# Optimization experiments

Measured on AMD Instinct MI355X. Metric: run time of the kernel, lower is better.

## Reference

```python
import jax, jax.numpy as jnp
import numpy as np

D_MODEL = 1024
N_HEADS = 16
D_HEAD = D_MODEL // N_HEADS
D_FF = 4 * D_MODEL
SEQ = 2048
BATCH = 4
EPS = 1e-5


def setup_inputs() -> dict:
    key = jax.random.key(0)
    ks = jax.random.split(key, 12)
    s = 0.02
    return {
        "x": jax.random.normal(ks[0], (BATCH, SEQ, D_MODEL), dtype=jnp.float32),
        "ln1_g": jnp.ones((D_MODEL,), jnp.float32),
        "ln1_b": jnp.zeros((D_MODEL,), jnp.float32),
        "wq": jax.random.normal(ks[1], (N_HEADS, D_MODEL, D_HEAD), jnp.float32) * s,
        "bq": jnp.zeros((N_HEADS, D_HEAD), jnp.float32),
        "wk": jax.random.normal(ks[2], (N_HEADS, D_MODEL, D_HEAD), jnp.float32) * s,
        "bk": jnp.zeros((N_HEADS, D_HEAD), jnp.float32),
        "wv": jax.random.normal(ks[3], (N_HEADS, D_MODEL, D_HEAD), jnp.float32) * s,
        "bv": jnp.zeros((N_HEADS, D_HEAD), jnp.float32),
        "wp": jax.random.normal(ks[4], (D_MODEL, D_MODEL), jnp.float32) * s,
        "bp": jnp.zeros((D_MODEL,), jnp.float32),
        "ln2_g": jnp.ones((D_MODEL,), jnp.float32),
        "ln2_b": jnp.zeros((D_MODEL,), jnp.float32),
        "w1": jax.random.normal(ks[5], (D_MODEL, D_FF), jnp.float32) * s,
        "b1": jnp.zeros((D_FF,), jnp.float32),
        "w2": jax.random.normal(ks[6], (D_FF, D_MODEL), jnp.float32) * s,
        "b2": jnp.zeros((D_MODEL,), jnp.float32),
    }


def _layer_norm(x, g, b):
    mu = jnp.mean(x, axis=-1, keepdims=True)
    var = jnp.mean(jnp.square(x - mu), axis=-1, keepdims=True)
    return (x - mu) * jax.lax.rsqrt(var + EPS) * g + b


def _block(x, ln1_g, ln1_b, wq, bq, wk, bk, wv, bv, wp, bp,
           ln2_g, ln2_b, w1, b1, w2, b2):
    B, S, D = x.shape
    # --- pre-LN multi-head causal self-attention ---
    xn = _layer_norm(x, ln1_g, ln1_b)
    q = jnp.einsum('bsd,hde->bhse', xn, wq) + bq[None, :, None, :]
    k = jnp.einsum('bsd,hde->bhse', xn, wk) + bk[None, :, None, :]
    v = jnp.einsum('bsd,hde->bhse', xn, wv) + bv[None, :, None, :]
    scores = jnp.einsum('bhse,bhte->bhst', q, k) / np.sqrt(D_HEAD).astype(np.float32)
    causal = jnp.tril(jnp.ones((S, S), dtype=bool))
    scores = jnp.where(causal[None, None], scores, jnp.float32(-jnp.inf))
    attn = jax.nn.softmax(scores, axis=-1)
    o = jnp.einsum('bhst,bhte->bhse', attn, v)          # [B,H,S,Dh]
    o = o.transpose(0, 2, 1, 3).reshape(B, S, D)         # concat heads
    x = x + o @ wp + bp
    # --- pre-LN feedforward ---
    xn2 = _layer_norm(x, ln2_g, ln2_b)
    h = jax.nn.relu(xn2 @ w1 + b1)
    x = x + h @ w2 + b2
    return x


def reference(x, ln1_g, ln1_b, wq, bq, wk, bk, wv, bv, wp, bp,
              ln2_g, ln2_b, w1, b1, w2, b2):
    return _block(x, ln1_g, ln1_b, wq, bq, wk, bk, wv, bv, wp, bp,
                  ln2_g, ln2_b, w1, b1, w2, b2)
```

## Files before the change

kernel.cpp:

```cpp
#include <hip/hip_runtime.h>
#include <hip/hip_bf16.h>

#define D_MODEL 1024
#define N_HEADS 16
#define D_HEAD  64
#define D_FF    4096
#define SEQ     2048
#define BATCH   4
#define NROWS   (BATCH * SEQ)

typedef __attribute__((ext_vector_type(8))) short short8;
typedef __attribute__((ext_vector_type(4))) float f32x4;

#define EXP2(x) exp2f(x)
#define MFMA16(a, b, c) __builtin_amdgcn_mfma_f32_16x16x32_bf16(a, b, c, 0, 0, 0)

static __device__ __forceinline__ ushort f2bf(float x) {
  __hip_bfloat16 h = __float2bfloat16(x);
  return *reinterpret_cast<ushort*>(&h);
}

static __device__ __forceinline__ void gl_lds16(const ushort* g, ushort* l) {
  __builtin_amdgcn_global_load_lds(
      (const __attribute__((address_space(1))) void*)g,
      (__attribute__((address_space(3))) void*)l, 16, 0, 0);
}

__global__ __launch_bounds__(256) void transpose_pack_b(
    const float* __restrict__ in, ushort* __restrict__ out,
    int K, int N, size_t in_bs, size_t out_bs) {
  in  += (size_t)blockIdx.z * in_bs;
  out += (size_t)blockIdx.z * out_bs;
  __shared__ float tile[32][33];
  int n0 = blockIdx.x * 32, k0 = blockIdx.y * 32;
  int tx = threadIdx.x, ty = threadIdx.y;
#pragma unroll
  for (int i = 0; i < 32; i += 8)
    tile[ty + i][tx] = in[(size_t)(k0 + ty + i) * N + n0 + tx];
  __syncthreads();
#pragma unroll
  for (int i = 0; i < 32; i += 8)
    out[(size_t)(n0 + ty + i) * K + k0 + tx] = f2bf(tile[tx][ty + i]);
}

__global__ __launch_bounds__(256) void transpose_v(
    const ushort* __restrict__ v, ushort* __restrict__ vt) {
  const int s0 = blockIdx.x * 64;
  const int bh = blockIdx.y, bb = bh >> 4, hh = bh & 15;
  __shared__ ushort tile[64][66];
  const ushort* src = v + (size_t)bb * SEQ * D_MODEL + (size_t)hh * 64;
  const int tx = threadIdx.x;
#pragma unroll
  for (int i = threadIdx.y; i < 64; i += 4)
    tile[i][tx] = src[(size_t)(s0 + i) * D_MODEL + tx];
  __syncthreads();
  ushort* dst = vt + (size_t)bh * 64 * SEQ + s0;
#pragma unroll
  for (int d = threadIdx.y; d < 64; d += 4)
    dst[(size_t)d * SEQ + tx] = tile[tx][d];
}

__global__ __launch_bounds__(256) void ln_kernel(
    const float* __restrict__ x, const float* __restrict__ g,
    const float* __restrict__ b, ushort* __restrict__ out) {
  int row = blockIdx.x, t = threadIdx.x;
  const float4 v = *(const float4*)(x + (size_t)row * D_MODEL + t * 4);
  float s  = v.x + v.y + v.z + v.w;
  float ss = v.x * v.x + v.y * v.y + v.z * v.z + v.w * v.w;
#pragma unroll
  for (int off = 1; off < 64; off <<= 1) {
    s  += __shfl_xor(s, off, 64);
    ss += __shfl_xor(ss, off, 64);
  }
  __shared__ float rs_[4], rss_[4];
  int w = t >> 6;
  if ((t & 63) == 0) { rs_[w] = s; rss_[w] = ss; }
  __syncthreads();
  s  = rs_[0] + rs_[1] + rs_[2] + rs_[3];
  ss = rss_[0] + rss_[1] + rss_[2] + rss_[3];
  float mu  = s * (1.0f / D_MODEL);
  float var = ss * (1.0f / D_MODEL) - mu * mu;
  float rstd = rsqrtf(var + 1e-5f);
  float4 gg = *(const float4*)(g + t * 4);
  float4 bb = *(const float4*)(b + t * 4);
  ushort4 r;
  r.x = f2bf((v.x - mu) * rstd * gg.x + bb.x);
  r.y = f2bf((v.y - mu) * rstd * gg.y + bb.y);
  r.z = f2bf((v.z - mu) * rstd * gg.z + bb.z);
  r.w = f2bf((v.w - mu) * rstd * gg.w + bb.w);
  *(ushort4*)(out + (size_t)row * D_MODEL + t * 4) = r;
}

template <int MODE>
__global__ __launch_bounds__(512, 2) void gemm256(
    const ushort* __restrict__ A, const ushort* __restrict__ BT,
    int M, int N, int K,
    const float* __restrict__ bias0, const float* __restrict__ bias1,
    const float* __restrict__ bias2,
    void* __restrict__ out0, void* __restrict__ out1, void* __restrict__ out2) {
  __shared__ __align__(16) ushort As[2][256 * 64];
  __shared__ __align__(16) ushort Bs[2][256 * 64];
  const int gx = N >> 8;
  const int nwg = gx * (M >> 8);
  const int cpx = nwg >> 3;
  const int tile = (blockIdx.x & 7) * cpx + (blockIdx.x >> 3);
  const int bn = tile % gx, bm = tile / gx;
  const int t = threadIdx.x, lane = t & 63, w = t >> 6;
  const int wr = w >> 2, wc = w & 3;
  const int l16 = lane & 15, l4 = lane >> 4;

  const ushort* Ab = A + (size_t)(bm * 256) * K;
  const ushort* Bb = BT + (size_t)(bn * 256) * K;

  int srow[4], scol[4];
#pragma unroll
  for (int i = 0; i < 4; ++i) {
    int c = i * 512 + t;
    srow[i] = c >> 3;
    scol[i] = 8 * ((c & 7) ^ ((c >> 3) & 7));
  }

  f32x4 acc[8][4] = {};
  int cur = 0;
  const int nk = K >> 6;

#pragma unroll
  for (int i = 0; i < 4; ++i) {
    gl_lds16(&Ab[(size_t)srow[i] * K + scol[i]], (ushort*)&As[0][(i * 512 + w * 64) * 8]);
    gl_lds16(&Bb[(size_t)srow[i] * K + scol[i]], (ushort*)&Bs[0][(i * 512 + w * 64) * 8]);
  }

  for (int kt = 0; kt < nk; ++kt) {
    if (kt + 1 < nk) {
      const int k0n = (kt + 1) << 6;
#pragma unroll
      for (int i = 0; i < 4; ++i) {
        gl_lds16(&Ab[(size_t)srow[i] * K + k0n + scol[i]], (ushort*)&As[cur ^ 1][(i * 512 + w * 64) * 8]);
        gl_lds16(&Bb[(size_t)srow[i] * K + k0n + scol[i]], (ushort*)&Bs[cur ^ 1][(i * 512 + w * 64) * 8]);
      }
      asm volatile("s_waitcnt vmcnt(8)" ::: "memory");
    } else {
      asm volatile("s_waitcnt vmcnt(0)" ::: "memory");
    }
    __builtin_amdgcn_s_barrier();

    const ushort* As_ = As[cur];
    const ushort* Bs_ = Bs[cur];
    short8 bfr[4][2];
#pragma unroll
    for (int n = 0; n < 4; ++n) {
      const int row = wc * 64 + n * 16 + l16;
      const int sw = (row & 7) * 8;
      bfr[n][0] = *(const short8*)&Bs_[row * 64 + ((l4 * 8) ^ sw)];
      bfr[n][1] = *(const short8*)&Bs_[row * 64 + ((l4 * 8 + 32) ^ sw)];
    }
#pragma unroll
    for (int m = 0; m < 8; ++m) {
      const int row = wr * 128 + m * 16 + l16;
      const int sw = (row & 7) * 8;
      short8 a0 = *(const short8*)&As_[row * 64 + ((l4 * 8) ^ sw)];
      short8 a1 = *(const short8*)&As_[row * 64 + ((l4 * 8 + 32) ^ sw)];
#pragma unroll
      for (int n = 0; n < 4; ++n) {
        acc[m][n] = MFMA16(a0, bfr[n][0], acc[m][n]);
        acc[m][n] = MFMA16(a1, bfr[n][1], acc[m][n]);
      }
    }
    asm volatile("" ::: "memory");
    __builtin_amdgcn_s_barrier();
    cur ^= 1;
  }

  const int row0 = bm * 256 + wr * 128, col0 = bn * 256 + wc * 64;
#pragma unroll
  for (int m = 0; m < 8; ++m) {
#pragma unroll
    for (int n = 0; n < 4; ++n) {
      const int col = col0 + n * 16 + l16;
      if (MODE == 0) {
        const int which = col >> 10;
        const int c = col & 1023;
        const float* bp_ = (which == 0) ? bias0 : (which == 1) ? bias1 : bias2;
        ushort* op = (which == 0) ? (ushort*)out0 : (which == 1) ? (ushort*)out1 : (ushort*)out2;
        const float scale = (which == 0) ? 0.125f * 1.44269504f : 1.0f;
#pragma unroll
        for (int i = 0; i < 4; ++i) {
          const int row = row0 + m * 16 + l4 * 4 + i;
          op[(size_t)row * D_MODEL + c] = f2bf((acc[m][n][i] + bp_[c]) * scale);
        }
      } else {
#pragma unroll
        for (int i = 0; i < 4; ++i) {
          const int row = row0 + m * 16 + l4 * 4 + i;
          const float val = fmaxf(acc[m][n][i] + bias0[col], 0.0f);
          ((ushort*)out0)[(size_t)row * D_FF + col] = f2bf(val);
        }
      }
    }
  }
}

__global__ __launch_bounds__(256, 2) void gemm128d(
    const ushort* __restrict__ A, const ushort* __restrict__ BT,
    int M, int N, int K,
    const float* __restrict__ bias0, const float* __restrict__ resid,
    float* __restrict__ out0) {
  __shared__ __align__(16) ushort As[2][128 * 64];
  __shared__ __align__(16) ushort Bs[2][128 * 64];
  const int gx = N >> 7;
  const int nwg = gx * (M >> 7);
  const int cpx = nwg >> 3;
  const int tile = (blockIdx.x & 7) * cpx + (blockIdx.x >> 3);
  const int bn = tile % gx, bm = tile / gx;
  const int t = threadIdx.x, lane = t & 63, w = t >> 6;
  const int wr = w >> 1, wc = w & 1;
  const int l16 = lane & 15, l4 = lane >> 4;

  const ushort* Ab = A + (size_t)(bm * 128) * K;
  const ushort* Bb = BT + (size_t)(bn * 128) * K;

  int srow[4], scol[4];
#pragma unroll
  for (int i = 0; i < 4; ++i) {
    int c = i * 256 + t;
    srow[i] = c >> 3;
    scol[i] = 8 * ((c & 7) ^ ((c >> 3) & 7));
  }

  f32x4 acc[4][4] = {};
  int cur = 0;
  const int nk = K >> 6;

#pragma unroll
  for (int i = 0; i < 4; ++i) {
    gl_lds16(&Ab[(size_t)srow[i] * K + scol[i]], (ushort*)&As[0][(i * 256 + w * 64) * 8]);
    gl_lds16(&Bb[(size_t)srow[i] * K + scol[i]], (ushort*)&Bs[0][(i * 256 + w * 64) * 8]);
  }

  for (int kt = 0; kt < nk; ++kt) {
    if (kt + 1 < nk) {
      const int k0n = (kt + 1) << 6;
#pragma unroll
      for (int i = 0; i < 4; ++i) {
        gl_lds16(&Ab[(size_t)srow[i] * K + k0n + scol[i]], (ushort*)&As[cur ^ 1][(i * 256 + w * 64) * 8]);
        gl_lds16(&Bb[(size_t)srow[i] * K + k0n + scol[i]], (ushort*)&Bs[cur ^ 1][(i * 256 + w * 64) * 8]);
      }
      asm volatile("s_waitcnt vmcnt(8)" ::: "memory");
    } else {
      asm volatile("s_waitcnt vmcnt(0)" ::: "memory");
    }
    __builtin_amdgcn_s_barrier();

    const ushort* As_ = As[cur];
    const ushort* Bs_ = Bs[cur];
    short8 bfr[4][2];
#pragma unroll
    for (int n = 0; n < 4; ++n) {
      const int row = wc * 64 + n * 16 + l16;
      const int sw = (row & 7) * 8;
      bfr[n][0] = *(const short8*)&Bs_[row * 64 + ((l4 * 8) ^ sw)];
      bfr[n][1] = *(const short8*)&Bs_[row * 64 + ((l4 * 8 + 32) ^ sw)];
    }
#pragma unroll
    for (int m = 0; m < 4; ++m) {
      const int row = wr * 64 + m * 16 + l16;
      const int sw = (row & 7) * 8;
      short8 a0 = *(const short8*)&As_[row * 64 + ((l4 * 8) ^ sw)];
      short8 a1 = *(const short8*)&As_[row * 64 + ((l4 * 8 + 32) ^ sw)];
#pragma unroll
      for (int n = 0; n < 4; ++n) {
        acc[m][n] = MFMA16(a0, bfr[n][0], acc[m][n]);
        acc[m][n] = MFMA16(a1, bfr[n][1], acc[m][n]);
      }
    }
    asm volatile("" ::: "memory");
    __builtin_amdgcn_s_barrier();
    cur ^= 1;
  }

  const int row0 = bm * 128 + wr * 64, col0 = bn * 128 + wc * 64;
#pragma unroll
  for (int m = 0; m < 4; ++m) {
#pragma unroll
    for (int n = 0; n < 4; ++n) {
      const int col = col0 + n * 16 + l16;
#pragma unroll
      for (int i = 0; i < 4; ++i) {
        const int row = row0 + m * 16 + l4 * 4 + i;
        const size_t idx = (size_t)row * D_MODEL + col;
        out0[idx] = acc[m][n][i] + bias0[col] + resid[idx];
      }
    }
  }
}

__global__ __launch_bounds__(256) void attn7_kernel(
    const ushort* __restrict__ Q, const ushort* __restrict__ Km,
    const ushort* __restrict__ Vt, ushort* __restrict__ O) {
  const int b = blockIdx.x;
  const int bh = (b & 7) * 8 + ((b >> 3) & 7);
  const int p = b >> 6;
  const int bb = bh >> 4, hh = bh & 15;
  const int t = threadIdx.x, lane = t & 63, w = t >> 6;
  const int l16 = lane & 15, l4 = lane >> 4;
  const size_t base  = (size_t)bb * SEQ * D_MODEL + (size_t)hh * 64;
  const size_t vbase = (size_t)bh * 64 * SEQ;

  __shared__ __align__(16) ushort Ks[2][64 * 64];
  __shared__ __align__(16) ushort Vs[2][64 * 64];
  __shared__ __align__(16) ushort Pw[4][32 * 64];
  ushort* myP = &Pw[w][0];

#define STAGE(ktile, buf) do {                                                     \
    const int kv0_ = (ktile) * 64;                                                 \
    _Pragma("unroll")                                                              \
    for (int i_ = 0; i_ < 2; ++i_) {                                               \
      const int g_ = i_ * 256 + t;                                                 \
      const int row_ = g_ >> 3;                                                    \
      const int c8_ = ((g_ & 7) ^ (row_ & 7)) * 8;                                 \
      gl_lds16(&Km[base + (size_t)(kv0_ + row_) * D_MODEL + c8_],                  \
               (ushort*)&Ks[buf][(i_ * 256 + w * 64) * 8]);                        \
      gl_lds16(&Vt[vbase + (size_t)row_ * SEQ + kv0_ + c8_],                       \
               (ushort*)&Vs[buf][(i_ * 256 + w * 64) * 8]);                        \
    }                                                                              \
  } while (0)

#pragma unroll
  for (int pan = 0; pan < 2; ++pan) {
    const int qt = pan ? p : (15 - p);
    const int qb = qt * 128 + w * 32;
    const int nt = qt * 2 + 2;

    short8 qf[2][2];
#pragma unroll
    for (int qj = 0; qj < 2; ++qj)
#pragma unroll
      for (int dk = 0; dk < 2; ++dk)
        qf[qj][dk] = *(const short8*)&Q[base + (size_t)(qb + qj * 16 + l16) * D_MODEL + dk * 32 + l4 * 8];

    f32x4 oacc[4][2] = {};
    float l_i[2] = {0.0f, 0.0f};

    STAGE(0, 0);

    int cur = 0;
    for (int kt = 0; kt < nt; ++kt) {
      const int kv0 = kt * 64;
      if (kt + 1 < nt) {
        STAGE(kt + 1, cur ^ 1);
        asm volatile("s_waitcnt vmcnt(4)" ::: "memory");
      } else {
        asm volatile("s_waitcnt vmcnt(0)" ::: "memory");
      }
      __builtin_amdgcn_s_barrier();

      const bool active = (kv0 <= qb + 31);
      if (active) {
        const ushort* Kc = Ks[cur];
        const ushort* Vc = Vs[cur];

        f32x4 sacc[2][4] = {};
#pragma unroll
        for (int n = 0; n < 4; ++n) {
          const int r = n * 16 + l16;
          const int rs = r * 8, rx = r & 7;
#pragma unroll
          for (int dk = 0; dk < 2; ++dk) {
            short8 ak = *(const short8*)&Kc[(rs + ((dk * 4 + l4) ^ rx)) * 8];
            sacc[0][n] = MFMA16(ak, qf[0][dk], sacc[0][n]);
            sacc[1][n] = MFMA16(ak, qf[1][dk], sacc[1][n]);
          }
        }

        const bool diag = (kv0 + 63 > qb);
#pragma unroll
        for (int qj = 0; qj < 2; ++qj) {
          const int qq = qb + qj * 16 + l16;
          const int ql = qj * 16 + l16;
          const int psw = (ql & 7) * 8;
          if (diag) {
#pragma unroll
            for (int n = 0; n < 4; ++n)
#pragma unroll
              for (int i = 0; i < 4; ++i) {
                const int kv = kv0 + n * 16 + l4 * 4 + i;
                if (kv > qq) sacc[qj][n][i] = -1e30f;
              }
          }
          float lsum = 0.0f;
#pragma unroll
          for (int n = 0; n < 4; ++n) {
            const float p0 = EXP2(sacc[qj][n][0]);
            const float p1 = EXP2(sacc[qj][n][1]);
            const float p2 = EXP2(sacc[qj][n][2]);
            const float p3 = EXP2(sacc[qj][n][3]);
            lsum += p0 + p1 + p2 + p3;
            ushort4 pk;
            pk.x = f2bf(p0); pk.y = f2bf(p1); pk.z = f2bf(p2); pk.w = f2bf(p3);
            *(ushort4*)&myP[ql * 64 + ((n * 16 + l4 * 4) ^ psw)] = pk;
          }
          l_i[qj] += lsum;
        }

#pragma unroll
        for (int kk = 0; kk < 2; ++kk) {
          short8 bp[2];
#pragma unroll
          for (int qj = 0; qj < 2; ++qj) {
            const int ql = qj * 16 + l16;
            bp[qj] = *(const short8*)&myP[ql * 64 + ((kk * 32 + l4 * 8) ^ ((ql & 7) * 8))];
          }
#pragma unroll
          for (int nd = 0; nd < 4; ++nd) {
            const int r = nd * 16 + l16;
            short8 av = *(const short8*)&Vc[(r * 8 + ((kk * 4 + l4) ^ (r & 7))) * 8];
            oacc[nd][0] = MFMA16(av, bp[0], oacc[nd][0]);
            oacc[nd][1] = MFMA16(av, bp[1], oacc[nd][1]);
          }
        }
      }

      asm volatile("" ::: "memory");
      __builtin_amdgcn_s_barrier();
      cur ^= 1;
    }

#pragma unroll
    for (int qj = 0; qj < 2; ++qj) {
      l_i[qj] += __shfl_xor(l_i[qj], 16, 64);
      l_i[qj] += __shfl_xor(l_i[qj], 32, 64);
      const int qq = qb + qj * 16 + l16;
      const float inv = 1.0f / l_i[qj];
#pragma unroll
      for (int nd = 0; nd < 4; ++nd) {
        ushort4 r;
        r.x = f2bf(oacc[nd][qj][0] * inv);
        r.y = f2bf(oacc[nd][qj][1] * inv);
        r.z = f2bf(oacc[nd][qj][2] * inv);
        r.w = f2bf(oacc[nd][qj][3] * inv);
        *(ushort4*)&O[base + (size_t)qq * D_MODEL + nd * 16 + l4 * 4] = r;
      }
    }
  }
#undef STAGE
}

extern "C" void kernel_launch(void* const* d_in, const int* in_sizes, int n_in,
                              void* d_out, int out_size, void* d_ws, size_t ws_size,
                              hipStream_t stream) {
  const float* x    = (const float*)d_in[0];
  const float* ln1g = (const float*)d_in[1];
  const float* ln1b = (const float*)d_in[2];
  const float* wq   = (const float*)d_in[3];
  const float* bq   = (const float*)d_in[4];
  const float* wk   = (const float*)d_in[5];
  const float* bk   = (const float*)d_in[6];
  const float* wv   = (const float*)d_in[7];
  const float* bv   = (const float*)d_in[8];
  const float* wp   = (const float*)d_in[9];
  const float* bp   = (const float*)d_in[10];
  const float* ln2g = (const float*)d_in[11];
  const float* ln2b = (const float*)d_in[12];
  const float* w1   = (const float*)d_in[13];
  const float* b1   = (const float*)d_in[14];
  const float* w2   = (const float*)d_in[15];
  const float* b2   = (const float*)d_in[16];
  float* out = (float*)d_out;

  char* base = (char*)d_ws;
  size_t off = 0;
  auto alloc = [&](size_t bytes) -> void* {
    void* r = base + off;
    off += (bytes + 255) & ~(size_t)255;
    return r;
  };
  ushort* WqkvT = (ushort*)alloc((size_t)3 * D_MODEL * D_MODEL * 2);
  ushort* WpT   = (ushort*)alloc((size_t)D_MODEL * D_MODEL * 2);
  ushort* W1T   = (ushort*)alloc((size_t)D_FF * D_MODEL * 2);
  ushort* W2T   = (ushort*)alloc((size_t)D_MODEL * D_FF * 2);
  ushort* xn    = (ushort*)alloc((size_t)NROWS * D_MODEL * 2);
  ushort* q     = (ushort*)alloc((size_t)NROWS * D_MODEL * 2);
  ushort* k     = (ushort*)alloc((size_t)NROWS * D_MODEL * 2);
  ushort* v     = (ushort*)alloc((size_t)NROWS * D_MODEL * 2);
  ushort* o     = (ushort*)alloc((size_t)NROWS * D_MODEL * 2);
  float*  x2    = (float*) alloc((size_t)NROWS * D_MODEL * 4);
  ushort* xn2   = (ushort*)alloc((size_t)NROWS * D_MODEL * 2);
  ushort* hbuf  = (ushort*)alloc((size_t)NROWS * D_FF * 2);
  ushort* vt = xn;

  dim3 tb(32, 8);
  transpose_pack_b<<<dim3(2, 32, 16), tb, 0, stream>>>(wq, WqkvT + (size_t)0 * D_MODEL * D_MODEL,
      D_MODEL, D_HEAD, (size_t)D_MODEL * D_HEAD, (size_t)D_HEAD * D_MODEL);
  transpose_pack_b<<<dim3(2, 32, 16), tb, 0, stream>>>(wk, WqkvT + (size_t)1 * D_MODEL * D_MODEL,
      D_MODEL, D_HEAD, (size_t)D_MODEL * D_HEAD, (size_t)D_HEAD * D_MODEL);
  transpose_pack_b<<<dim3(2, 32, 16), tb, 0, stream>>>(wv, WqkvT + (size_t)2 * D_MODEL * D_MODEL,
      D_MODEL, D_HEAD, (size_t)D_MODEL * D_HEAD, (size_t)D_HEAD * D_MODEL);
  transpose_pack_b<<<dim3(32, 32, 1), tb, 0, stream>>>(wp, WpT, D_MODEL, D_MODEL, 0, 0);
  transpose_pack_b<<<dim3(128, 32, 1), tb, 0, stream>>>(w1, W1T, D_MODEL, D_FF, 0, 0);
  transpose_pack_b<<<dim3(32, 128, 1), tb, 0, stream>>>(w2, W2T, D_FF, D_MODEL, 0, 0);

  ln_kernel<<<NROWS, 256, 0, stream>>>(x, ln1g, ln1b, xn);
  gemm256<0><<<dim3((NROWS / 256) * (3 * D_MODEL / 256)), 512, 0, stream>>>(
      xn, WqkvT, NROWS, 3 * D_MODEL, D_MODEL, bq, bk, bv, q, k, v);
  transpose_v<<<dim3(SEQ / 64, BATCH * N_HEADS), dim3(64, 4), 0, stream>>>(v, vt);
  attn7_kernel<<<512, 256, 0, stream>>>(q, k, vt, o);
  gemm128d<<<dim3((NROWS / 128) * (D_MODEL / 128)), 256, 0, stream>>>(
      o, WpT, NROWS, D_MODEL, D_MODEL, bp, x, x2);
  ln_kernel<<<NROWS, 256, 0, stream>>>(x2, ln2g, ln2b, xn2);
  gemm256<2><<<dim3((NROWS / 256) * (D_FF / 256)), 512, 0, stream>>>(
      xn2, W1T, NROWS, D_FF, D_MODEL, b1, nullptr, nullptr, hbuf, nullptr, nullptr);
  gemm128d<<<dim3((NROWS / 128) * (D_MODEL / 128)), 256, 0, stream>>>(
      hbuf, W2T, NROWS, D_MODEL, D_FF, b2, x2, out);
}
```

Measured before the change: 376.5 us.

## Write V transposed from QKV GEMM epilogue and prefetch two KV tiles ahead

The QKV GEMM epilogue now writes V directly in per-head transposed [b,h,d,s] layout with ushort4 stores, which removes the separate transpose_v kernel and its extra round trip of V through memory. The attention kernel grows its K/V LDS buffers from two to four stages and processes key tiles in pairs, issuing loads two tiles ahead with a single barrier pair per two tiles. This doubles the K/V LDS footprint, which may reduce occupancy. The transposed V stores from the GEMM are strided across rows and may be less coalesced.

```diff
diff --git a/kernel.cpp b/kernel.cpp
--- a/kernel.cpp
+++ b/kernel.cpp
@@ -41,23 +41,6 @@
 #pragma unroll
   for (int i = 0; i < 32; i += 8)
     out[(size_t)(n0 + ty + i) * K + k0 + tx] = f2bf(tile[tx][ty + i]);
-}
-
-__global__ __launch_bounds__(256) void transpose_v(
-    const ushort* __restrict__ v, ushort* __restrict__ vt) {
-  const int s0 = blockIdx.x * 64;
-  const int bh = blockIdx.y, bb = bh >> 4, hh = bh & 15;
-  __shared__ ushort tile[64][66];
-  const ushort* src = v + (size_t)bb * SEQ * D_MODEL + (size_t)hh * 64;
-  const int tx = threadIdx.x;
-#pragma unroll
-  for (int i = threadIdx.y; i < 64; i += 4)
-    tile[i][tx] = src[(size_t)(s0 + i) * D_MODEL + tx];
-  __syncthreads();
-  ushort* dst = vt + (size_t)bh * 64 * SEQ + s0;
-#pragma unroll
-  for (int d = threadIdx.y; d < 64; d += 4)
-    dst[(size_t)d * SEQ + tx] = tile[tx][d];
 }
 
 __global__ __launch_bounds__(256) void ln_kernel(
@@ -180,13 +163,26 @@
       if (MODE == 0) {
         const int which = col >> 10;
         const int c = col & 1023;
-        const float* bp_ = (which == 0) ? bias0 : (which == 1) ? bias1 : bias2;
-        ushort* op = (which == 0) ? (ushort*)out0 : (which == 1) ? (ushort*)out1 : (ushort*)out2;
-        const float scale = (which == 0) ? 0.125f * 1.44269504f : 1.0f;
-#pragma unroll
-        for (int i = 0; i < 4; ++i) {
-          const int row = row0 + m * 16 + l4 * 4 + i;
-          op[(size_t)row * D_MODEL + c] = f2bf((acc[m][n][i] + bp_[c]) * scale);
+        if (which < 2) {
+          const float* bp_ = (which == 0) ? bias0 : bias1;
+          ushort* op = (which == 0) ? (ushort*)out0 : (ushort*)out1;
+          const float scale = (which == 0) ? 0.125f * 1.44269504f : 1.0f;
+#pragma unroll
+          for (int i = 0; i < 4; ++i) {
+            const int row = row0 + m * 16 + l4 * 4 + i;
+            op[(size_t)row * D_MODEL + c] = f2bf((acc[m][n][i] + bp_[c]) * scale);
+          }
+        } else {
+          const int d = c & 63, hh2 = c >> 6;
+          const float bv_ = bias2[c];
+          ushort4 r4;
+          r4.x = f2bf(acc[m][n][0] + bv_);
+          r4.y = f2bf(acc[m][n][1] + bv_);
+          r4.z = f2bf(acc[m][n][2] + bv_);
+          r4.w = f2bf(acc[m][n][3] + bv_);
+          const int row = row0 + m * 16 + l4 * 4;
+          const int bb2 = row >> 11, s = row & 2047;
+          *(ushort4*)((ushort*)out2 + ((size_t)(bb2 * 16 + hh2) * 64 + d) * SEQ + s) = r4;
         }
       } else {
 #pragma unroll
@@ -294,7 +290,7 @@
   }
 }
 
-__global__ __launch_bounds__(256) void attn7_kernel(
+__global__ __launch_bounds__(256) void attn8_kernel(
     const ushort* __restrict__ Q, const ushort* __restrict__ Km,
     const ushort* __restrict__ Vt, ushort* __restrict__ O) {
   const int b = blockIdx.x;
@@ -306,8 +302,8 @@
   const size_t base  = (size_t)bb * SEQ * D_MODEL + (size_t)hh * 64;
   const size_t vbase = (size_t)bh * 64 * SEQ;
 
-  __shared__ __align__(16) ushort Ks[2][64 * 64];
-  __shared__ __align__(16) ushort Vs[2][64 * 64];
+  __shared__ __align__(16) ushort Ks[4][64 * 64];
+  __shared__ __align__(16) ushort Vs[4][64 * 64];
   __shared__ __align__(16) ushort Pw[4][32 * 64];
   ushort* myP = &Pw[w][0];
 
@@ -342,87 +338,91 @@
     float l_i[2] = {0.0f, 0.0f};
 
     STAGE(0, 0);
-
-    int cur = 0;
-    for (int kt = 0; kt < nt; ++kt) {
-      const int kv0 = kt * 64;
-      if (kt + 1 < nt) {
-        STAGE(kt + 1, cur ^ 1);
-        asm volatile("s_waitcnt vmcnt(4)" ::: "memory");
+    STAGE(1, 1);
+
+    for (int jt = 0; jt < nt; jt += 2) {
+      if (jt + 2 < nt) {
+        STAGE(jt + 2, (jt + 2) & 3);
+        STAGE(jt + 3, (jt + 3) & 3);
+        asm volatile("s_waitcnt vmcnt(8)" ::: "memory");
       } else {
         asm volatile("s_waitcnt vmcnt(0)" ::: "memory");
       }
       __builtin_amdgcn_s_barrier();
 
-      const bool active = (kv0 <= qb + 31);
-      if (active) {
-        const ushort* Kc = Ks[cur];
-        const ushort* Vc = Vs[cur];
-
-        f32x4 sacc[2][4] = {};
-#pragma unroll
-        for (int n = 0; n < 4; ++n) {
-          const int r = n * 16 + l16;
-          const int rs = r * 8, rx = r & 7;
-#pragma unroll
-          for (int dk = 0; dk < 2; ++dk) {
-            short8 ak = *(const short8*)&Kc[(rs + ((dk * 4 + l4) ^ rx)) * 8];
-            sacc[0][n] = MFMA16(ak, qf[0][dk], sacc[0][n]);
-            sacc[1][n] = MFMA16(ak, qf[1][dk], sacc[1][n]);
+#pragma unroll
+      for (int half = 0; half < 2; ++half) {
+        const int kt = jt + half;
+        const int kv0 = kt * 64;
+        const bool active = (kv0 <= qb + 31);
+        if (active) {
+          const ushort* Kc = Ks[kt & 3];
+          const ushort* Vc = Vs[kt & 3];
+
+          f32x4 sacc[2][4] = {};
+#pragma unroll
+          for (int n = 0; n < 4; ++n) {
+            const int r = n * 16 + l16;
+            const int rs = r * 8, rx = r & 7;
+#pragma unroll
+            for (int dk = 0; dk < 2; ++dk) {
+              short8 ak = *(const short8*)&Kc[(rs + ((dk * 4 + l4) ^ rx)) * 8];
+              sacc[0][n] = MFMA16(ak, qf[0][dk], sacc[0][n]);
+              sacc[1][n] = MFMA16(ak, qf[1][dk], sacc[1][n]);
+            }
+          }
+
+          const bool diag = (kv0 + 63 > qb);
+#pragma unroll
+          for (int qj = 0; qj < 2; ++qj) {
+            const int qq = qb + qj * 16 + l16;
+            const int ql = qj * 16 + l16;
+            const int psw = (ql & 7) * 8;
+            if (diag) {
+#pragma unroll
+              for (int n = 0; n < 4; ++n)
+#pragma unroll
+                for (int i = 0; i < 4; ++i) {
+                  const int kv = kv0 + n * 16 + l4 * 4 + i;
+                  if (kv > qq) sacc[qj][n][i] = -1e30f;
+                }
+            }
+            float lsum = 0.0f;
+#pragma unroll
+            for (int n = 0; n < 4; ++n) {
+              const float p0 = EXP2(sacc[qj][n][0]);
+              const float p1 = EXP2(sacc[qj][n][1]);
+              const float p2 = EXP2(sacc[qj][n][2]);
+              const float p3 = EXP2(sacc[qj][n][3]);
+              lsum += p0 + p1 + p2 + p3;
+              ushort4 pk;
+              pk.x = f2bf(p0); pk.y = f2bf(p1); pk.z = f2bf(p2); pk.w = f2bf(p3);
+              *(ushort4*)&myP[ql * 64 + ((n * 16 + l4 * 4) ^ psw)] = pk;
+            }
+            l_i[qj] += lsum;
+          }
+
+#pragma unroll
+          for (int kk = 0; kk < 2; ++kk) {
+            short8 bp[2];
+#pragma unroll
+            for (int qj = 0; qj < 2; ++qj) {
+              const int ql = qj * 16 + l16;
+              bp[qj] = *(const short8*)&myP[ql * 64 + ((kk * 32 + l4 * 8) ^ ((ql & 7) * 8))];
+            }
+#pragma unroll
+            for (int nd = 0; nd < 4; ++nd) {
+              const int r = nd * 16 + l16;
+              short8 av = *(const short8*)&Vc[(r * 8 + ((kk * 4 + l4) ^ (r & 7))) * 8];
+              oacc[nd][0] = MFMA16(av, bp[0], oacc[nd][0]);
+              oacc[nd][1] = MFMA16(av, bp[1], oacc[nd][1]);
+            }
           }
         }
-
-        const bool diag = (kv0 + 63 > qb);
-#pragma unroll
-        for (int qj = 0; qj < 2; ++qj) {
-          const int qq = qb + qj * 16 + l16;
-          const int ql = qj * 16 + l16;
-          const int psw = (ql & 7) * 8;
-          if (diag) {
-#pragma unroll
-            for (int n = 0; n < 4; ++n)
-#pragma unroll
-              for (int i = 0; i < 4; ++i) {
-                const int kv = kv0 + n * 16 + l4 * 4 + i;
-                if (kv > qq) sacc[qj][n][i] = -1e30f;
-              }
-          }
-          float lsum = 0.0f;
-#pragma unroll
-          for (int n = 0; n < 4; ++n) {
-            const float p0 = EXP2(sacc[qj][n][0]);
-            const float p1 = EXP2(sacc[qj][n][1]);
-            const float p2 = EXP2(sacc[qj][n][2]);
-            const float p3 = EXP2(sacc[qj][n][3]);
-            lsum += p0 + p1 + p2 + p3;
-            ushort4 pk;
-            pk.x = f2bf(p0); pk.y = f2bf(p1); pk.z = f2bf(p2); pk.w = f2bf(p3);
-            *(ushort4*)&myP[ql * 64 + ((n * 16 + l4 * 4) ^ psw)] = pk;
-          }
-          l_i[qj] += lsum;
-        }
-
-#pragma unroll
-        for (int kk = 0; kk < 2; ++kk) {
-          short8 bp[2];
-#pragma unroll
-          for (int qj = 0; qj < 2; ++qj) {
-            const int ql = qj * 16 + l16;
-            bp[qj] = *(const short8*)&myP[ql * 64 + ((kk * 32 + l4 * 8) ^ ((ql & 7) * 8))];
-          }
-#pragma unroll
-          for (int nd = 0; nd < 4; ++nd) {
-            const int r = nd * 16 + l16;
-            short8 av = *(const short8*)&Vc[(r * 8 + ((kk * 4 + l4) ^ (r & 7))) * 8];
-            oacc[nd][0] = MFMA16(av, bp[0], oacc[nd][0]);
-            oacc[nd][1] = MFMA16(av, bp[1], oacc[nd][1]);
-          }
-        }
       }
 
       asm volatile("" ::: "memory");
       __builtin_amdgcn_s_barrier();
-      cur ^= 1;
     }
 
 #pragma unroll
@@ -481,12 +481,11 @@
   ushort* xn    = (ushort*)alloc((size_t)NROWS * D_MODEL * 2);
   ushort* q     = (ushort*)alloc((size_t)NROWS * D_MODEL * 2);
   ushort* k     = (ushort*)alloc((size_t)NROWS * D_MODEL * 2);
-  ushort* v     = (ushort*)alloc((size_t)NROWS * D_MODEL * 2);
+  ushort* vt    = (ushort*)alloc((size_t)NROWS * D_MODEL * 2);
   ushort* o     = (ushort*)alloc((size_t)NROWS * D_MODEL * 2);
   float*  x2    = (float*) alloc((size_t)NROWS * D_MODEL * 4);
   ushort* xn2   = (ushort*)alloc((size_t)NROWS * D_MODEL * 2);
   ushort* hbuf  = (ushort*)alloc((size_t)NROWS * D_FF * 2);
-  ushort* vt = xn;
 
   dim3 tb(32, 8);
   transpose_pack_b<<<dim3(2, 32, 16), tb, 0, stream>>>(wq, WqkvT + (size_t)0 * D_MODEL * D_MODEL,
@@ -501,9 +500,8 @@
 
   ln_kernel<<<NROWS, 256, 0, stream>>>(x, ln1g, ln1b, xn);
   gemm256<0><<<dim3((NROWS / 256) * (3 * D_MODEL / 256)), 512, 0, stream>>>(
-      xn, WqkvT, NROWS, 3 * D_MODEL, D_MODEL, bq, bk, bv, q, k, v);
-  transpose_v<<<dim3(SEQ / 64, BATCH * N_HEADS), dim3(64, 4), 0, stream>>>(v, vt);
-  attn7_kernel<<<512, 256, 0, stream>>>(q, k, vt, o);
+      xn, WqkvT, NROWS, 3 * D_MODEL, D_MODEL, bq, bk, bv, q, k, vt);
+  attn8_kernel<<<512, 256, 0, stream>>>(q, k, vt, o);
   gemm128d<<<dim3((NROWS / 128) * (D_MODEL / 128)), 256, 0, stream>>>(
       o, WpT, NROWS, D_MODEL, D_MODEL, bp, x, x2);
   ln_kernel<<<NROWS, 256, 0, stream>>>(x2, ln2g, ln2b, xn2);
```

Result: faster. 362.8 us (-3.6%).
